# Optimization experiments

Measured on AMD Instinct MI355X. Metric: run time of the kernel, lower is better.

## Reference

```python
import jax, jax.numpy as jnp
import numpy as np


def setup_inputs() -> dict:
    key = jax.random.key(0)
    ks = jax.random.split(key, 9)
    B, Cr, H, W = 16, 1024, 28, 28
    Cs, Hs, Ws = 256, 25, 25  # Hs == Ws so adaptive pool == mean over width
    Ci = 512
    return {
        "x_rgb": jax.random.normal(ks[0], (B, Cr, H, W), jnp.float32),
        "x_skel": jax.random.normal(ks[1], (B, Cs, Hs, Ws), jnp.float32),
        "Wq": jax.random.normal(ks[2], (Ci, Cr), jnp.float32) * (Cr ** -0.5),
        "bq": jax.random.normal(ks[3], (Ci,), jnp.float32) * 0.01,
        "Wk": jax.random.normal(ks[4], (Ci, Cs), jnp.float32) * (Cs ** -0.5),
        "bk": jax.random.normal(ks[5], (Ci,), jnp.float32) * 0.01,
        "Wv": jax.random.normal(ks[6], (Cr, Cs), jnp.float32) * (Cs ** -0.5),
        "bv": jax.random.normal(ks[7], (Cr,), jnp.float32) * 0.01,
        "gamma": jax.random.normal(ks[8], (1,), jnp.float32) * 0.1,
    }


def reference(x_rgb, x_skel, Wq, bq, Wk, bk, Wv, bv, gamma):
    B, Cr, H, W = x_rgb.shape
    Ws = x_skel.shape[3]
    # adaptive_avg_pool2d(x_skel, (Ws, 1)) with Hs == Ws -> mean over width
    pooled = jnp.mean(x_skel, axis=3)  # [B, Cs, Ws]
    # 1x1 conv projections as matmuls
    q = jnp.einsum('ic,bchw->bihw', Wq, x_rgb) + bq[None, :, None, None]
    q = q.reshape(B, -1, H * W).transpose(0, 2, 1)          # [B, HW, Ci]
    k = jnp.einsum('ic,bcs->bis', Wk, pooled) + bk[None, :, None]  # [B, Ci, Ws]
    energy = jnp.einsum('bni,bis->bns', q, k)               # [B, HW, Ws]
    attention = jax.nn.softmax(energy, axis=-1)             # [B, HW, Ws]
    v = jnp.einsum('rc,bcs->brs', Wv, pooled) + bv[None, :, None]  # [B, Cr, Ws]
    out = jnp.einsum('brs,bns->brn', v, attention)          # [B, Cr, HW]
    out = out.reshape(B, Cr, H, W)
    return gamma[0] * out + x_rgb
```

## Files before the change

kernel.cpp:

```cpp
#include <hip/hip_runtime.h>

#define BB 16
#define CR 1024
#define HWD 784
#define HW2 392
#define CS 256
#define SSZ 25
#define SP 28
#define CI 512
#define NBLK 512

#define OFF_VP     102400
#define OFF_MP     561152
#define OFF_E0     1019904
#define OFF_KK     1333904
#define OFF_BAR    3842704

#define NGRP  32
#define GRPSZ 16
#define BAR_UINTS 1040

__device__ __forceinline__ void gbar(unsigned* bar, unsigned phase) {
    __syncthreads();
    if (threadIdx.x < 64) {
        const unsigned g = (unsigned)blockIdx.x >> 4;
        const int lane = threadIdx.x;
        unsigned tk = 0;
        if (lane == 0) {
            __builtin_amdgcn_fence(__ATOMIC_RELEASE, "agent");
            unsigned a = __hip_atomic_fetch_add(bar + g * 16, 1u,
                           __ATOMIC_RELAXED, __HIP_MEMORY_SCOPE_AGENT);
            if (a == phase * GRPSZ - 1)
                tk = 1u + __hip_atomic_fetch_add(bar + 512, 1u,
                             __ATOMIC_RELAXED, __HIP_MEMORY_SCOPE_AGENT);
        }
        tk = __shfl(tk, 0);
        if (tk == phase * NGRP && lane < NGRP)
            __hip_atomic_fetch_add(bar + 528 + lane * 16, 1u,
                                   __ATOMIC_RELAXED, __HIP_MEMORY_SCOPE_AGENT);
        if (lane == 0) {
            const unsigned* gen = bar + 528 + g * 16;
            int spins = 0;
            while (__hip_atomic_load(gen, __ATOMIC_RELAXED,
                                     __HIP_MEMORY_SCOPE_AGENT) != phase) {
                __builtin_amdgcn_s_sleep(4);
                if (++spins > (1 << 22)) break;
            }
            __builtin_amdgcn_fence(__ATOMIC_ACQUIRE, "agent");
        }
    }
    __syncthreads();
}

template <int NS>
__device__ __forceinline__ void proj_body(const float* __restrict__ wrow,
                                          const float* __restrict__ pb, int s0,
                                          float bias, float* __restrict__ dst,
                                          bool zpad) {
    float acc[NS];
#pragma unroll
    for (int i = 0; i < NS; ++i) acc[i] = 0.f;
    const float4* w4 = (const float4*)wrow;
#pragma unroll 4
    for (int c4 = 0; c4 < CS / 4; ++c4) {
        float4 w = w4[c4];
        const float* p = pb + c4 * 4 * SSZ + s0;
#pragma unroll
        for (int i = 0; i < NS; ++i)
            acc[i] = fmaf(w.x, p[i],
                     fmaf(w.y, p[SSZ + i],
                     fmaf(w.z, p[2 * SSZ + i],
                     fmaf(w.w, p[3 * SSZ + i], acc[i]))));
    }
#pragma unroll
    for (int i = 0; i < NS; ++i) dst[s0 + i] = acc[i] + bias;
    if (zpad) { dst[25] = 0.f; dst[26] = 0.f; dst[27] = 0.f; }
}

__global__ __launch_bounds__(256, 2) void mega(
    const float* __restrict__ xr, const float* __restrict__ xs,
    const float* __restrict__ Wq, const float* __restrict__ bq,
    const float* __restrict__ Wk, const float* __restrict__ bk,
    const float* __restrict__ Wv, const float* __restrict__ bv,
    const float* __restrict__ gm, float* __restrict__ out,
    float* __restrict__ ws)
{
    __shared__ __align__(16) float lds[13600];

    float* vp     = ws + OFF_VP;
    float* Mp     = ws + OFF_MP;
    float* e0     = ws + OFF_E0;
    float* kk     = ws + OFF_KK;
    unsigned* bar = (unsigned*)(ws + OFF_BAR);

    const int tid  = threadIdx.x;
    const int wave = tid >> 6, lane = tid & 63;
    const int bid  = blockIdx.x;

    {
        int b = bid >> 5, slot = bid & 31;
        if (slot < 24) {
            const float* xsb = xs + (size_t)b * CS * SSZ * SSZ;
#pragma unroll
            for (int q = 0; q < 25; ++q) {
                int e = tid + 256 * q;
                const float* row = xsb + (size_t)e * SSZ;
                float s = 0.f;
#pragma unroll
                for (int w = 0; w < SSZ; ++w) s += row[w];
                lds[e] = s * (1.0f / SSZ);
            }
            __syncthreads();
            int rb = slot >> 2, sh = slot & 3;
            const float* wrow; float bias; float* dst;
            if (rb < 2) {
                int i = rb * 256 + tid;
                wrow = Wk + (size_t)i * CS; bias = bk[i];
                dst  = kk + ((size_t)b * CI + i) * SP;
            } else {
                int r = (rb - 2) * 256 + tid;
                wrow = Wv + (size_t)r * CS; bias = bv[r];
                dst  = vp + ((size_t)b * CR + r) * SP;
            }
            int s0 = sh * 7;
            if (sh < 3) proj_body<7>(wrow, lds, s0, bias, dst, false);
            else        proj_body<4>(wrow, lds, s0, bias, dst, true);
        }
    }
    gbar(bar, 1);

    if (bid < 416) {
        int sc = bid % 13, rem = bid / 13;
        int b = rem >> 1, chalf = rem & 1;
        int s0 = sc * 2;
        float* kst = lds;
        float* red = lds + 1024;
        const float* kkb = kk + (size_t)b * CI * SP;
#pragma unroll
        for (int q = 0; q < 4; ++q) {
            int d = tid + 256 * q;
            kst[d] = kkb[(size_t)(d >> 1) * SP + s0 + (d & 1)];
        }
        __syncthreads();
        int half = tid >> 7, tq = tid & 127;
        int cq = chalf * 512 + 4 * tq;
        float acc[8];
#pragma unroll
        for (int e = 0; e < 8; ++e) acc[e] = 0.f;
        const float2* kst2 = (const float2*)kst;
        int i0 = half * 256;
#pragma unroll 4
        for (int i = 0; i < 256; ++i) {
            float4 w = *(const float4*)(Wq + (size_t)(i0 + i) * CR + cq);
            float2 k = kst2[i0 + i];
#pragma unroll
            for (int cl = 0; cl < 4; ++cl) {
                float wc = cl == 0 ? w.x : cl == 1 ? w.y : cl == 2 ? w.z : w.w;
                acc[cl * 2 + 0] = fmaf(wc, k.x, acc[cl * 2 + 0]);
                acc[cl * 2 + 1] = fmaf(wc, k.y, acc[cl * 2 + 1]);
            }
        }
        if (half == 1) {
#pragma unroll
            for (int j = 0; j < 8; ++j) red[tq * 9 + j] = acc[j];
        }
        __syncthreads();
        if (half == 0) {
#pragma unroll
            for (int j = 0; j < 8; ++j) acc[j] += red[tq * 9 + j];
#pragma unroll
            for (int cl = 0; cl < 4; ++cl) {
                float2 o = make_float2(acc[cl * 2 + 0], acc[cl * 2 + 1]);
                *(float2*)&Mp[((size_t)(b << 10) + cq + cl) * SP + s0] = o;
            }
        }
    } else if (bid >= 448) {
        int wt0 = (bid - 448) * 4 + wave;
        for (int wt = wt0; wt < 400; wt += 256) {
            int s = wt % 25, b = wt / 25;
            const float* kb = kk + (size_t)b * CI * SP;
            float a = 0.f;
#pragma unroll
            for (int k = 0; k < CI / 64; ++k) {
                int i = lane + 64 * k;
                a = fmaf(bq[i], kb[(size_t)i * SP + s], a);
            }
#pragma unroll
            for (int off = 32; off > 0; off >>= 1) a += __shfl_down(a, off);
            if (lane == 0) e0[b * SSZ + s] = a;
        }
    }
    gbar(bar, 2);

    if (bid < 25 * BB) {
        int tile = bid % 25, b = bid / 25;
        int cg = tid >> 4, nl = tid & 15;
        int n2 = tile * 16 + nl;
        bool valid = n2 < HW2;
        int n2c = valid ? n2 : 0;
        const float2* x2 = (const float2*)(xr + (size_t)b * CR * HWD);

        float a0[SSZ], a1[SSZ];
#pragma unroll
        for (int s = 0; s < SSZ; ++s) { a0[s] = 0.f; a1[s] = 0.f; }
        const int c0 = cg * 64;
        for (int c = c0; c < c0 + 64; c += 4) {
            float2 xv[4];
#pragma unroll
            for (int u = 0; u < 4; ++u)
                xv[u] = x2[(size_t)(c + u) * HW2 + n2c];
#pragma unroll
            for (int u = 0; u < 4; ++u) {
                const float4* mr = (const float4*)&Mp[((size_t)(b << 10) + c + u) * SP];
#pragma unroll
                for (int j = 0; j < 6; ++j) {
                    float4 m = mr[j];
                    a0[4 * j + 0] = fmaf(xv[u].x, m.x, a0[4 * j + 0]);
                    a0[4 * j + 1] = fmaf(xv[u].x, m.y, a0[4 * j + 1]);
                    a0[4 * j + 2] = fmaf(xv[u].x, m.z, a0[4 * j + 2]);
                    a0[4 * j + 3] = fmaf(xv[u].x, m.w, a0[4 * j + 3]);
                    a1[4 * j + 0] = fmaf(xv[u].y, m.x, a1[4 * j + 0]);
                    a1[4 * j + 1] = fmaf(xv[u].y, m.y, a1[4 * j + 1]);
                    a1[4 * j + 2] = fmaf(xv[u].y, m.z, a1[4 * j + 2]);
                    a1[4 * j + 3] = fmaf(xv[u].y, m.w, a1[4 * j + 3]);
                }
                float m24 = mr[6].x;
                a0[24] = fmaf(xv[u].x, m24, a0[24]);
                a1[24] = fmaf(xv[u].y, m24, a1[24]);
            }
        }
        float2* part = (float2*)lds;
#pragma unroll
        for (int s = 0; s < SSZ; ++s) part[tid * SSZ + s] = make_float2(a0[s], a1[s]);
        __syncthreads();

        float2* att2 = part + 6400;
        if (tid < 16) {
            float ex[SSZ], ey[SSZ];
#pragma unroll
            for (int s = 0; s < SSZ; ++s) { float v = e0[b * SSZ + s]; ex[s] = v; ey[s] = v; }
            for (int g16 = 0; g16 < 16; ++g16) {
#pragma unroll
                for (int s = 0; s < SSZ; ++s) {
                    float2 p = part[(g16 * 16 + tid) * SSZ + s];
                    ex[s] += p.x; ey[s] += p.y;
                }
            }
            float mx = ex[0], my = ey[0];
#pragma unroll
            for (int s = 1; s < SSZ; ++s) { mx = fmaxf(mx, ex[s]); my = fmaxf(my, ey[s]); }
            float sx = 0.f, sy = 0.f;
#pragma unroll
            for (int s = 0; s < SSZ; ++s) {
                ex[s] = __expf(ex[s] - mx); sx += ex[s];
                ey[s] = __expf(ey[s] - my); sy += ey[s];
            }
            float ix = 1.0f / sx, iy = 1.0f / sy;
#pragma unroll
            for (int s = 0; s < SSZ; ++s)
                att2[tid * SSZ + s] = make_float2(ex[s] * ix, ey[s] * iy);
        }
        __syncthreads();

#pragma unroll
        for (int s = 0; s < SSZ; ++s) {
            float2 av = att2[nl * SSZ + s];
            a0[s] = av.x; a1[s] = av.y;
        }
        float g = gm[0];
        float2* o2 = (float2*)(out + (size_t)b * CR * HWD);
        const int r0 = cg * 64;
        for (int r = r0; r < r0 + 64; r += 2) {
            float2 xva = x2[(size_t)r * HW2 + n2c];
            float2 xvb = x2[(size_t)(r + 1) * HW2 + n2c];
            const float4* vra = (const float4*)&vp[((size_t)(b << 10) + r) * SP];
            const float4* vrb = (const float4*)&vp[((size_t)(b << 10) + r + 1) * SP];
            float d0a = 0.f, d1a = 0.f, d0b = 0.f, d1b = 0.f;
#pragma unroll
            for (int j = 0; j < 6; ++j) {
                float4 va = vra[j], vb = vrb[j];
                d0a = fmaf(va.x, a0[4 * j + 0], d0a);
                d0a = fmaf(va.y, a0[4 * j + 1], d0a);
                d0a = fmaf(va.z, a0[4 * j + 2], d0a);
                d0a = fmaf(va.w, a0[4 * j + 3], d0a);
                d1a = fmaf(va.x, a1[4 * j + 0], d1a);
                d1a = fmaf(va.y, a1[4 * j + 1], d1a);
                d1a = fmaf(va.z, a1[4 * j + 2], d1a);
                d1a = fmaf(va.w, a1[4 * j + 3], d1a);
                d0b = fmaf(vb.x, a0[4 * j + 0], d0b);
                d0b = fmaf(vb.y, a0[4 * j + 1], d0b);
                d0b = fmaf(vb.z, a0[4 * j + 2], d0b);
                d0b = fmaf(vb.w, a0[4 * j + 3], d0b);
                d1b = fmaf(vb.x, a1[4 * j + 0], d1b);
                d1b = fmaf(vb.y, a1[4 * j + 1], d1b);
                d1b = fmaf(vb.z, a1[4 * j + 2], d1b);
                d1b = fmaf(vb.w, a1[4 * j + 3], d1b);
            }
            d0a = fmaf(vra[6].x, a0[24], d0a);
            d1a = fmaf(vra[6].x, a1[24], d1a);
            d0b = fmaf(vrb[6].x, a0[24], d0b);
            d1b = fmaf(vrb[6].x, a1[24], d1b);
            if (valid) {
                o2[(size_t)r * HW2 + n2] =
                    make_float2(fmaf(g, d0a, xva.x), fmaf(g, d1a, xva.y));
                o2[(size_t)(r + 1) * HW2 + n2] =
                    make_float2(fmaf(g, d0b, xvb.x), fmaf(g, d1b, xvb.y));
            }
        }
    }
}

extern "C" void kernel_launch(void* const* d_in, const int* in_sizes, int n_in,
                              void* d_out, int out_size, void* d_ws, size_t ws_size,
                              hipStream_t stream) {
    const float* x_rgb  = (const float*)d_in[0];
    const float* x_skel = (const float*)d_in[1];
    const float* Wq     = (const float*)d_in[2];
    const float* bq     = (const float*)d_in[3];
    const float* Wk     = (const float*)d_in[4];
    const float* bk     = (const float*)d_in[5];
    const float* Wv     = (const float*)d_in[6];
    const float* bv     = (const float*)d_in[7];
    const float* gamma  = (const float*)d_in[8];
    float* out = (float*)d_out;
    float* ws  = (float*)d_ws;

    hipMemsetAsync(ws + OFF_BAR, 0, BAR_UINTS * sizeof(unsigned), stream);

    hipLaunchKernelGGL(mega, dim3(NBLK), dim3(256), 0, stream,
                       x_rgb, x_skel, Wq, bq, Wk, bk, Wv, bv, gamma, out, ws);
}
```

Measured before the change: 287.1 us.

## Replace grid-wide barriers with per-batch XCD-local work queues and counters

Removes the two global grid barriers. Each block now reads its XCC id from a hardware register and serves two batches mapped to that XCD, taking tasks for each stage from per-batch atomic queues and waiting only on per-batch completion counters. The intent is to keep each batch's intermediate data in one XCD's L2 and let batches progress independently instead of stalling on the whole grid. The Mp stage also now computes 4 s-columns per task instead of 2, which halves the number of Wq passes. The risks are load imbalance if blocks are unevenly spread across XCDs, extra atomic traffic, and a spin-wait that depends on all blocks being co-resident.

Measured after the change: 264.6 us. 1.09x faster.

```diff
diff --git a/kernel.cpp b/kernel.cpp
--- a/kernel.cpp
+++ b/kernel.cpp
@@ -14,42 +14,15 @@
 #define OFF_MP     561152
 #define OFF_E0     1019904
 #define OFF_KK     1333904
-#define OFF_BAR    3842704
-
-#define NGRP  32
-#define GRPSZ 16
-#define BAR_UINTS 1040
-
-__device__ __forceinline__ void gbar(unsigned* bar, unsigned phase) {
-    __syncthreads();
-    if (threadIdx.x < 64) {
-        const unsigned g = (unsigned)blockIdx.x >> 4;
-        const int lane = threadIdx.x;
-        unsigned tk = 0;
-        if (lane == 0) {
-            __builtin_amdgcn_fence(__ATOMIC_RELEASE, "agent");
-            unsigned a = __hip_atomic_fetch_add(bar + g * 16, 1u,
-                           __ATOMIC_RELAXED, __HIP_MEMORY_SCOPE_AGENT);
-            if (a == phase * GRPSZ - 1)
-                tk = 1u + __hip_atomic_fetch_add(bar + 512, 1u,
-                             __ATOMIC_RELAXED, __HIP_MEMORY_SCOPE_AGENT);
-        }
-        tk = __shfl(tk, 0);
-        if (tk == phase * NGRP && lane < NGRP)
-            __hip_atomic_fetch_add(bar + 528 + lane * 16, 1u,
-                                   __ATOMIC_RELAXED, __HIP_MEMORY_SCOPE_AGENT);
-        if (lane == 0) {
-            const unsigned* gen = bar + 528 + g * 16;
-            int spins = 0;
-            while (__hip_atomic_load(gen, __ATOMIC_RELAXED,
-                                     __HIP_MEMORY_SCOPE_AGENT) != phase) {
-                __builtin_amdgcn_s_sleep(4);
-                if (++spins > (1 << 22)) break;
-            }
-            __builtin_amdgcn_fence(__ATOMIC_ACQUIRE, "agent");
-        }
-    }
-    __syncthreads();
+#define OFF_CTR    2000000
+#define CTR_UINTS  (88 * 16)
+
+
+__device__ __forceinline__ unsigned rmw_inc(unsigned* p) {
+    return __hip_atomic_fetch_add(p, 1u, __ATOMIC_RELAXED, __HIP_MEMORY_SCOPE_AGENT);
+}
+__device__ __forceinline__ unsigned aload(const unsigned* p) {
+    return __hip_atomic_load(p, __ATOMIC_RELAXED, __HIP_MEMORY_SCOPE_AGENT);
 }
 
 template <int NS>
@@ -86,20 +59,37 @@
     float* __restrict__ ws)
 {
     __shared__ __align__(16) float lds[13600];
+    __shared__ unsigned comm;
 
     float* vp     = ws + OFF_VP;
     float* Mp     = ws + OFF_MP;
     float* e0     = ws + OFF_E0;
     float* kk     = ws + OFF_KK;
-    unsigned* bar = (unsigned*)(ws + OFF_BAR);
+    unsigned* ctr = (unsigned*)(ws + OFF_CTR);
 
     const int tid  = threadIdx.x;
     const int wave = tid >> 6, lane = tid & 63;
-    const int bid  = blockIdx.x;
-
-    {
-        int b = bid >> 5, slot = bid & 31;
-        if (slot < 24) {
+
+    const unsigned xcc = __builtin_amdgcn_s_getreg(20 | (0 << 6) | (3 << 11)) & 7u;
+
+    if (tid == 0) comm = rmw_inc(ctr + xcc * 16);
+    __syncthreads();
+    const unsigned pref = comm & 1u;
+
+    for (int pass = 0; pass < 2; ++pass) {
+        const int b = 2 * (int)xcc + (int)(pref ^ (unsigned)pass);
+        unsigned* tA = ctr + (8  + b) * 16;
+        unsigned* dA = ctr + (24 + b) * 16;
+        unsigned* tB = ctr + (40 + b) * 16;
+        unsigned* dB = ctr + (56 + b) * 16;
+        unsigned* tF = ctr + (72 + b) * 16;
+
+        for (;;) {
+            __syncthreads();
+            if (tid == 0) comm = rmw_inc(tA);
+            __syncthreads();
+            unsigned t = comm;
+            if (t >= 24) break;
             const float* xsb = xs + (size_t)b * CS * SSZ * SSZ;
 #pragma unroll
             for (int q = 0; q < 25; ++q) {
@@ -111,7 +101,7 @@
                 lds[e] = s * (1.0f / SSZ);
             }
             __syncthreads();
-            int rb = slot >> 2, sh = slot & 3;
+            int rb = (int)t >> 2, sh = (int)t & 3;
             const float* wrow; float bias; float* dst;
             if (rb < 2) {
                 int i = rb * 256 + tid;
@@ -125,186 +115,218 @@
             int s0 = sh * 7;
             if (sh < 3) proj_body<7>(wrow, lds, s0, bias, dst, false);
             else        proj_body<4>(wrow, lds, s0, bias, dst, true);
-        }
-    }
-    gbar(bar, 1);
-
-    if (bid < 416) {
-        int sc = bid % 13, rem = bid / 13;
-        int b = rem >> 1, chalf = rem & 1;
-        int s0 = sc * 2;
-        float* kst = lds;
-        float* red = lds + 1024;
-        const float* kkb = kk + (size_t)b * CI * SP;
-#pragma unroll
-        for (int q = 0; q < 4; ++q) {
-            int d = tid + 256 * q;
-            kst[d] = kkb[(size_t)(d >> 1) * SP + s0 + (d & 1)];
+            __syncthreads();
+            if (tid == 0) rmw_inc(dA);
         }
         __syncthreads();
-        int half = tid >> 7, tq = tid & 127;
-        int cq = chalf * 512 + 4 * tq;
-        float acc[8];
-#pragma unroll
-        for (int e = 0; e < 8; ++e) acc[e] = 0.f;
-        const float2* kst2 = (const float2*)kst;
-        int i0 = half * 256;
+        if (tid == 0) {
+            int spins = 0;
+            while (aload(dA) < 24u) {
+                __builtin_amdgcn_s_sleep(8);
+                if (++spins > (1 << 18)) break;
+            }
+        }
+        __syncthreads();
+
+        for (;;) {
+            __syncthreads();
+            if (tid == 0) comm = rmw_inc(tB);
+            __syncthreads();
+            unsigned t = comm;
+            if (t >= 15) break;
+            if (t < 14) {
+                int sc = (int)t % 7, chalf = (int)t / 7;
+                int s0 = sc * 4;
+                float* kst = lds;
+                float* red = lds + 2048;
+                const float* kkb = kk + (size_t)b * CI * SP;
+#pragma unroll
+                for (int q = 0; q < 8; ++q) {
+                    int d = tid + 256 * q;
+                    kst[d] = kkb[(size_t)(d >> 2) * SP + s0 + (d & 3)];
+                }
+                __syncthreads();
+                int half = tid >> 7, tq = tid & 127;
+                int cq = chalf * 512 + 4 * tq;
+                float acc[16];
+#pragma unroll
+                for (int e = 0; e < 16; ++e) acc[e] = 0.f;
+                const float4* kst4 = (const float4*)kst;
+                int i0 = half * 256;
 #pragma unroll 4
-        for (int i = 0; i < 256; ++i) {
-            float4 w = *(const float4*)(Wq + (size_t)(i0 + i) * CR + cq);
-            float2 k = kst2[i0 + i];
-#pragma unroll
-            for (int cl = 0; cl < 4; ++cl) {
-                float wc = cl == 0 ? w.x : cl == 1 ? w.y : cl == 2 ? w.z : w.w;
-                acc[cl * 2 + 0] = fmaf(wc, k.x, acc[cl * 2 + 0]);
-                acc[cl * 2 + 1] = fmaf(wc, k.y, acc[cl * 2 + 1]);
-            }
-        }
-        if (half == 1) {
-#pragma unroll
-            for (int j = 0; j < 8; ++j) red[tq * 9 + j] = acc[j];
+                for (int i = 0; i < 256; ++i) {
+                    float4 w = *(const float4*)(Wq + (size_t)(i0 + i) * CR + cq);
+                    float4 k = kst4[i0 + i];
+#pragma unroll
+                    for (int cl = 0; cl < 4; ++cl) {
+                        float wc = cl == 0 ? w.x : cl == 1 ? w.y : cl == 2 ? w.z : w.w;
+                        acc[cl * 4 + 0] = fmaf(wc, k.x, acc[cl * 4 + 0]);
+                        acc[cl * 4 + 1] = fmaf(wc, k.y, acc[cl * 4 + 1]);
+                        acc[cl * 4 + 2] = fmaf(wc, k.z, acc[cl * 4 + 2]);
+                        acc[cl * 4 + 3] = fmaf(wc, k.w, acc[cl * 4 + 3]);
+                    }
+                }
+                if (half == 1) {
+#pragma unroll
+                    for (int j = 0; j < 16; ++j) red[tq * 17 + j] = acc[j];
+                }
+                __syncthreads();
+                if (half == 0) {
+#pragma unroll
+                    for (int j = 0; j < 16; ++j) acc[j] += red[tq * 17 + j];
+#pragma unroll
+                    for (int cl = 0; cl < 4; ++cl) {
+                        float4 o;
+                        o.x = acc[cl * 4 + 0]; o.y = acc[cl * 4 + 1];
+                        o.z = acc[cl * 4 + 2]; o.w = acc[cl * 4 + 3];
+                        *(float4*)&Mp[((size_t)(b << 10) + cq + cl) * SP + s0] = o;
+                    }
+                }
+            } else {
+                const float* kb = kk + (size_t)b * CI * SP;
+                for (int s = wave; s < SSZ; s += 4) {
+                    float a = 0.f;
+#pragma unroll
+                    for (int k2 = 0; k2 < CI / 64; ++k2) {
+                        int i = lane + 64 * k2;
+                        a = fmaf(bq[i], kb[(size_t)i * SP + s], a);
+                    }
+#pragma unroll
+                    for (int off = 32; off > 0; off >>= 1) a += __shfl_down(a, off);
+                    if (lane == 0) e0[b * SSZ + s] = a;
+                }
+            }
+            __syncthreads();
+            if (tid == 0) rmw_inc(dB);
         }
         __syncthreads();
-        if (half == 0) {
-#pragma unroll
-            for (int j = 0; j < 8; ++j) acc[j] += red[tq * 9 + j];
-#pragma unroll
-            for (int cl = 0; cl < 4; ++cl) {
-                float2 o = make_float2(acc[cl * 2 + 0], acc[cl * 2 + 1]);
-                *(float2*)&Mp[((size_t)(b << 10) + cq + cl) * SP + s0] = o;
-            }
-        }
-    } else if (bid >= 448) {
-        int wt0 = (bid - 448) * 4 + wave;
-        for (int wt = wt0; wt < 400; wt += 256) {
-            int s = wt % 25, b = wt / 25;
-            const float* kb = kk + (size_t)b * CI * SP;
-            float a = 0.f;
-#pragma unroll
-            for (int k = 0; k < CI / 64; ++k) {
-                int i = lane + 64 * k;
-                a = fmaf(bq[i], kb[(size_t)i * SP + s], a);
-            }
-#pragma unroll
-            for (int off = 32; off > 0; off >>= 1) a += __shfl_down(a, off);
-            if (lane == 0) e0[b * SSZ + s] = a;
-        }
-    }
-    gbar(bar, 2);
-
-    if (bid < 25 * BB) {
-        int tile = bid % 25, b = bid / 25;
-        int cg = tid >> 4, nl = tid & 15;
-        int n2 = tile * 16 + nl;
-        bool valid = n2 < HW2;
-        int n2c = valid ? n2 : 0;
-        const float2* x2 = (const float2*)(xr + (size_t)b * CR * HWD);
-
-        float a0[SSZ], a1[SSZ];
-#pragma unroll
-        for (int s = 0; s < SSZ; ++s) { a0[s] = 0.f; a1[s] = 0.f; }
-        const int c0 = cg * 64;
-        for (int c = c0; c < c0 + 64; c += 4) {
-            float2 xv[4];
-#pragma unroll
-            for (int u = 0; u < 4; ++u)
-                xv[u] = x2[(size_t)(c + u) * HW2 + n2c];
-#pragma unroll
-            for (int u = 0; u < 4; ++u) {
-                const float4* mr = (const float4*)&Mp[((size_t)(b << 10) + c + u) * SP];
+        if (tid == 0) {
+            int spins = 0;
+            while (aload(dB) < 15u) {
+                __builtin_amdgcn_s_sleep(8);
+                if (++spins > (1 << 18)) break;
+            }
+        }
+        __syncthreads();
+
+        for (;;) {
+            __syncthreads();
+            if (tid == 0) comm = rmw_inc(tF);
+            __syncthreads();
+            unsigned t = comm;
+            if (t >= 25) break;
+            int cg = tid >> 4, nl = tid & 15;
+            int n2 = (int)t * 16 + nl;
+            bool valid = n2 < HW2;
+            int n2c = valid ? n2 : 0;
+            const float2* x2 = (const float2*)(xr + (size_t)b * CR * HWD);
+
+            float a0[SSZ], a1[SSZ];
+#pragma unroll
+            for (int s = 0; s < SSZ; ++s) { a0[s] = 0.f; a1[s] = 0.f; }
+            const int c0 = cg * 64;
+            for (int c = c0; c < c0 + 64; c += 4) {
+                float2 xv[4];
+#pragma unroll
+                for (int u = 0; u < 4; ++u)
+                    xv[u] = x2[(size_t)(c + u) * HW2 + n2c];
+#pragma unroll
+                for (int u = 0; u < 4; ++u) {
+                    const float4* mr = (const float4*)&Mp[((size_t)(b << 10) + c + u) * SP];
+#pragma unroll
+                    for (int j = 0; j < 6; ++j) {
+                        float4 m = mr[j];
+                        a0[4 * j + 0] = fmaf(xv[u].x, m.x, a0[4 * j + 0]);
+                        a0[4 * j + 1] = fmaf(xv[u].x, m.y, a0[4 * j + 1]);
+                        a0[4 * j + 2] = fmaf(xv[u].x, m.z, a0[4 * j + 2]);
+                        a0[4 * j + 3] = fmaf(xv[u].x, m.w, a0[4 * j + 3]);
+                        a1[4 * j + 0] = fmaf(xv[u].y, m.x, a1[4 * j + 0]);
+                        a1[4 * j + 1] = fmaf(xv[u].y, m.y, a1[4 * j + 1]);
+                        a1[4 * j + 2] = fmaf(xv[u].y, m.z, a1[4 * j + 2]);
+                        a1[4 * j + 3] = fmaf(xv[u].y, m.w, a1[4 * j + 3]);
+                    }
+                    float m24 = mr[6].x;
+                    a0[24] = fmaf(xv[u].x, m24, a0[24]);
+                    a1[24] = fmaf(xv[u].y, m24, a1[24]);
+                }
+            }
+            float2* part = (float2*)lds;
+#pragma unroll
+            for (int s = 0; s < SSZ; ++s) part[tid * SSZ + s] = make_float2(a0[s], a1[s]);
+            __syncthreads();
+
+            float2* att2 = part + 6400;
+            if (tid < 16) {
+                float ex[SSZ], ey[SSZ];
+#pragma unroll
+                for (int s = 0; s < SSZ; ++s) { float v = e0[b * SSZ + s]; ex[s] = v; ey[s] = v; }
+                for (int g16 = 0; g16 < 16; ++g16) {
+#pragma unroll
+                    for (int s = 0; s < SSZ; ++s) {
+                        float2 p = part[(g16 * 16 + tid) * SSZ + s];
+                        ex[s] += p.x; ey[s] += p.y;
+                    }
+                }
+                float mx = ex[0], my = ey[0];
+#pragma unroll
+                for (int s = 1; s < SSZ; ++s) { mx = fmaxf(mx, ex[s]); my = fmaxf(my, ey[s]); }
+                float sx = 0.f, sy = 0.f;
+#pragma unroll
+                for (int s = 0; s < SSZ; ++s) {
+                    ex[s] = __expf(ex[s] - mx); sx += ex[s];
+                    ey[s] = __expf(ey[s] - my); sy += ey[s];
+                }
+                float ix = 1.0f / sx, iy = 1.0f / sy;
+#pragma unroll
+                for (int s = 0; s < SSZ; ++s)
+                    att2[tid * SSZ + s] = make_float2(ex[s] * ix, ey[s] * iy);
+            }
+            __syncthreads();
+
+#pragma unroll
+            for (int s = 0; s < SSZ; ++s) {
+                float2 av = att2[nl * SSZ + s];
+                a0[s] = av.x; a1[s] = av.y;
+            }
+            float g = gm[0];
+            float2* o2 = (float2*)(out + (size_t)b * CR * HWD);
+            const int r0 = cg * 64;
+            for (int r = r0; r < r0 + 64; r += 2) {
+                float2 xva = x2[(size_t)r * HW2 + n2c];
+                float2 xvb = x2[(size_t)(r + 1) * HW2 + n2c];
+                const float4* vra = (const float4*)&vp[((size_t)(b << 10) + r) * SP];
+                const float4* vrb = (const float4*)&vp[((size_t)(b << 10) + r + 1) * SP];
+                float d0a = 0.f, d1a = 0.f, d0b = 0.f, d1b = 0.f;
 #pragma unroll
                 for (int j = 0; j < 6; ++j) {
-                    float4 m = mr[j];
-                    a0[4 * j + 0] = fmaf(xv[u].x, m.x, a0[4 * j + 0]);
-                    a0[4 * j + 1] = fmaf(xv[u].x, m.y, a0[4 * j + 1]);
-                    a0[4 * j + 2] = fmaf(xv[u].x, m.z, a0[4 * j + 2]);
-                    a0[4 * j + 3] = fmaf(xv[u].x, m.w, a0[4 * j + 3]);
-                    a1[4 * j + 0] = fmaf(xv[u].y, m.x, a1[4 * j + 0]);
-                    a1[4 * j + 1] = fmaf(xv[u].y, m.y, a1[4 * j + 1]);
-                    a1[4 * j + 2] = fmaf(xv[u].y, m.z, a1[4 * j + 2]);
-                    a1[4 * j + 3] = fmaf(xv[u].y, m.w, a1[4 * j + 3]);
-                }
-                float m24 = mr[6].x;
-                a0[24] = fmaf(xv[u].x, m24, a0[24]);
-                a1[24] = fmaf(xv[u].y, m24, a1[24]);
-            }
-        }
-        float2* part = (float2*)lds;
-#pragma unroll
-        for (int s = 0; s < SSZ; ++s) part[tid * SSZ + s] = make_float2(a0[s], a1[s]);
-        __syncthreads();
-
-        float2* att2 = part + 6400;
-        if (tid < 16) {
-            float ex[SSZ], ey[SSZ];
-#pragma unroll
-            for (int s = 0; s < SSZ; ++s) { float v = e0[b * SSZ + s]; ex[s] = v; ey[s] = v; }
-            for (int g16 = 0; g16 < 16; ++g16) {
-#pragma unroll
-                for (int s = 0; s < SSZ; ++s) {
-                    float2 p = part[(g16 * 16 + tid) * SSZ + s];
-                    ex[s] += p.x; ey[s] += p.y;
-                }
-            }
-            float mx = ex[0], my = ey[0];
-#pragma unroll
-            for (int s = 1; s < SSZ; ++s) { mx = fmaxf(mx, ex[s]); my = fmaxf(my, ey[s]); }
-            float sx = 0.f, sy = 0.f;
-#pragma unroll
-            for (int s = 0; s < SSZ; ++s) {
-                ex[s] = __expf(ex[s] - mx); sx += ex[s];
-                ey[s] = __expf(ey[s] - my); sy += ey[s];
-            }
-            float ix = 1.0f / sx, iy = 1.0f / sy;
-#pragma unroll
-            for (int s = 0; s < SSZ; ++s)
-                att2[tid * SSZ + s] = make_float2(ex[s] * ix, ey[s] * iy);
-        }
-        __syncthreads();
-
-#pragma unroll
-        for (int s = 0; s < SSZ; ++s) {
-            float2 av = att2[nl * SSZ + s];
-            a0[s] = av.x; a1[s] = av.y;
-        }
-        float g = gm[0];
-        float2* o2 = (float2*)(out + (size_t)b * CR * HWD);
-        const int r0 = cg * 64;
-        for (int r = r0; r < r0 + 64; r += 2) {
-            float2 xva = x2[(size_t)r * HW2 + n2c];
-            float2 xvb = x2[(size_t)(r + 1) * HW2 + n2c];
-            const float4* vra = (const float4*)&vp[((size_t)(b << 10) + r) * SP];
-            const float4* vrb = (const float4*)&vp[((size_t)(b << 10) + r + 1) * SP];
-            float d0a = 0.f, d1a = 0.f, d0b = 0.f, d1b = 0.f;
-#pragma unroll
-            for (int j = 0; j < 6; ++j) {
-                float4 va = vra[j], vb = vrb[j];
-                d0a = fmaf(va.x, a0[4 * j + 0], d0a);
-                d0a = fmaf(va.y, a0[4 * j + 1], d0a);
-                d0a = fmaf(va.z, a0[4 * j + 2], d0a);
-                d0a = fmaf(va.w, a0[4 * j + 3], d0a);
-                d1a = fmaf(va.x, a1[4 * j + 0], d1a);
-                d1a = fmaf(va.y, a1[4 * j + 1], d1a);
-                d1a = fmaf(va.z, a1[4 * j + 2], d1a);
-                d1a = fmaf(va.w, a1[4 * j + 3], d1a);
-                d0b = fmaf(vb.x, a0[4 * j + 0], d0b);
-                d0b = fmaf(vb.y, a0[4 * j + 1], d0b);
-                d0b = fmaf(vb.z, a0[4 * j + 2], d0b);
-                d0b = fmaf(vb.w, a0[4 * j + 3], d0b);
-                d1b = fmaf(vb.x, a1[4 * j + 0], d1b);
-                d1b = fmaf(vb.y, a1[4 * j + 1], d1b);
-                d1b = fmaf(vb.z, a1[4 * j + 2], d1b);
-                d1b = fmaf(vb.w, a1[4 * j + 3], d1b);
-            }
-            d0a = fmaf(vra[6].x, a0[24], d0a);
-            d1a = fmaf(vra[6].x, a1[24], d1a);
-            d0b = fmaf(vrb[6].x, a0[24], d0b);
-            d1b = fmaf(vrb[6].x, a1[24], d1b);
-            if (valid) {
-                o2[(size_t)r * HW2 + n2] =
-                    make_float2(fmaf(g, d0a, xva.x), fmaf(g, d1a, xva.y));
-                o2[(size_t)(r + 1) * HW2 + n2] =
-                    make_float2(fmaf(g, d0b, xvb.x), fmaf(g, d1b, xvb.y));
+                    float4 va = vra[j], vb = vrb[j];
+                    d0a = fmaf(va.x, a0[4 * j + 0], d0a);
+                    d0a = fmaf(va.y, a0[4 * j + 1], d0a);
+                    d0a = fmaf(va.z, a0[4 * j + 2], d0a);
+                    d0a = fmaf(va.w, a0[4 * j + 3], d0a);
+                    d1a = fmaf(va.x, a1[4 * j + 0], d1a);
+                    d1a = fmaf(va.y, a1[4 * j + 1], d1a);
+                    d1a = fmaf(va.z, a1[4 * j + 2], d1a);
+                    d1a = fmaf(va.w, a1[4 * j + 3], d1a);
+                    d0b = fmaf(vb.x, a0[4 * j + 0], d0b);
+                    d0b = fmaf(vb.y, a0[4 * j + 1], d0b);
+                    d0b = fmaf(vb.z, a0[4 * j + 2], d0b);
+                    d0b = fmaf(vb.w, a0[4 * j + 3], d0b);
+                    d1b = fmaf(vb.x, a1[4 * j + 0], d1b);
+                    d1b = fmaf(vb.y, a1[4 * j + 1], d1b);
+                    d1b = fmaf(vb.z, a1[4 * j + 2], d1b);
+                    d1b = fmaf(vb.w, a1[4 * j + 3], d1b);
+                }
+                d0a = fmaf(vra[6].x, a0[24], d0a);
+                d1a = fmaf(vra[6].x, a1[24], d1a);
+                d0b = fmaf(vrb[6].x, a0[24], d0b);
+                d1b = fmaf(vrb[6].x, a1[24], d1b);
+                if (valid) {
+                    o2[(size_t)r * HW2 + n2] =
+                        make_float2(fmaf(g, d0a, xva.x), fmaf(g, d1a, xva.y));
+                    o2[(size_t)(r + 1) * HW2 + n2] =
+                        make_float2(fmaf(g, d0b, xvb.x), fmaf(g, d1b, xvb.y));
+                }
             }
         }
     }
@@ -325,7 +347,7 @@
     float* out = (float*)d_out;
     float* ws  = (float*)d_ws;
 
-    hipMemsetAsync(ws + OFF_BAR, 0, BAR_UINTS * sizeof(unsigned), stream);
+    hipMemsetAsync(ws + OFF_CTR, 0, CTR_UINTS * sizeof(unsigned), stream);
 
     hipLaunchKernelGGL(mega, dim3(NBLK), dim3(256), 0, stream,
                        x_rgb, x_skel, Wq, bq, Wk, bk, Wv, bv, gamma, out, ws);
```
